# Performance work log

Measured on AMD Instinct MI355X. Metric: run time of the kernel, lower is better.

## Reference

```python
import jax, jax.numpy as jnp
import numpy as np

NUM_HEADS = 8
KERNEL = 7
LOW_RANK = 4


def setup_inputs() -> dict:
    key = jax.random.key(0)
    ks = jax.random.split(key, 10)
    B, H, W, C = 4, 56, 56, 256
    nh, K, lr = NUM_HEADS, KERNEL, LOW_RANK
    s = 0.02
    return {
        "x": jax.random.normal(ks[0], (B, H, W, C), jnp.float32),
        "Wq": jax.random.normal(ks[1], (C, nh * lr), jnp.float32) * s,
        "bq": jnp.zeros((nh * lr,), jnp.float32),
        "Wk": jax.random.normal(ks[2], (C, nh * lr), jnp.float32) * s,
        "bk": jnp.zeros((nh * lr,), jnp.float32),
        "Wv": jax.random.normal(ks[3], (C, C), jnp.float32) * s,
        "bv": jnp.zeros((C,), jnp.float32),
        "rpb": jax.random.normal(ks[4], (nh, 2 * K - 1, 2 * K - 1), jnp.float32) * s,
        "Wp": jax.random.normal(ks[5], (C, C), jnp.float32) * s,
        "bp": jnp.zeros((C,), jnp.float32),
    }


def reference(x, Wq, bq, Wk, bk, Wv, bv, rpb, Wp, bp):
    B, H, W, C = x.shape
    nh, K, lr = NUM_HEADS, KERNEL, LOW_RANK
    hd = C // nh
    r = K // 2
    scale = hd ** -0.5

    # Projections. Note: the original uses a raw reshape (B,H,W,nh*lr)->(B,nh,H,W,lr),
    # which we replicate exactly (row-major reshape, no permute).
    q = (x @ Wq + bq).reshape(B, nh, H, W, lr) * scale
    k = (x @ Wk + bk).reshape(B, nh, H, W, lr)
    v = (x @ Wv + bv).reshape(B, nh, H, W, hd)

    # NATTEN window start indices (clamped so each query sees exactly K keys per axis).
    start_h = jnp.clip(jnp.arange(H) - r, 0, H - K)  # (H,)
    start_w = jnp.clip(jnp.arange(W) - r, 0, W - K)  # (W,)
    idx_h = start_h[:, None] + jnp.arange(K)[None, :]  # (H, K)
    idx_w = start_w[:, None] + jnp.arange(K)[None, :]  # (W, K)

    # Gather local K/V windows: (B, nh, H, K, W, K, d)
    k_win = k[:, :, idx_h][:, :, :, :, idx_w]
    v_win = v[:, :, idx_h][:, :, :, :, idx_w]

    # Scores: (B, nh, H, W, K, K)
    attn = jnp.einsum('bhijc,bhikjlc->bhijkl', q, k_win)

    # Relative position bias indices: (key_pos - query_pos) + (K-1)
    bi = idx_h - jnp.arange(H)[:, None] + (K - 1)  # (H, K)
    bj = idx_w - jnp.arange(W)[:, None] + (K - 1)  # (W, K)
    bias = rpb[:, bi][:, :, :, bj]                 # (nh, H, K, W, K)
    attn = attn + bias.transpose(0, 1, 3, 2, 4)[None]  # (B, nh, H, W, K, K)

    attn = jax.nn.softmax(attn.reshape(B, nh, H, W, K * K), axis=-1)
    attn = attn.reshape(B, nh, H, W, K, K)

    # Weighted aggregation of V windows: (B, nh, H, W, hd)
    out = jnp.einsum('bhijkl,bhikjld->bhijd', attn, v_win)
    out = out.transpose(0, 2, 3, 1, 4).reshape(B, H, W, C)
    return out @ Wp + bp
```

## Files before the change

kernel.cpp:

```cpp
#include <hip/hip_runtime.h>
#include <hip/hip_bf16.h>

#define BD 4
#define HD_ 56
#define WD 56
#define CD 256
#define NH 8
#define KW 7
#define LR 4
#define HDIM 32
#define MB (HD_*WD)
#define NROWS (BD*MB)
#define QK_PER_B (HD_*WD*32)
#define V_PER_B  (HD_*WD*256)

typedef short short8 __attribute__((ext_vector_type(8)));
typedef float floatx4 __attribute__((ext_vector_type(4)));

static __device__ inline ushort f2bf(float f) {
    __hip_bfloat16 h = __float2bfloat16(f);
    return *(ushort*)&h;
}

__global__ __launch_bounds__(256) void prep_w(
    const float* __restrict__ Wq, const float* __restrict__ Wk,
    const float* __restrict__ Wv, const float* __restrict__ bq,
    const float* __restrict__ bk, const float* __restrict__ bv,
    const float* __restrict__ Wp,
    ushort* __restrict__ WpkT, ushort* __restrict__ WpT, float* __restrict__ pb)
{
    int idx = blockIdx.x * 256 + threadIdx.x;
    if (idx < 81920) {
        int n = idx >> 8, k = idx & 255;
        float v;
        if (n < 32)       v = Wq[k * 32 + n];
        else if (n < 64)  v = Wk[k * 32 + (n - 32)];
        else              v = Wv[k * 256 + (n - 64)];
        WpkT[idx] = f2bf(v);
    } else if (idx < 81920 + 65536) {
        int j = idx - 81920;
        int n = j >> 8, k = j & 255;
        WpT[j] = f2bf(Wp[k * 256 + n]);
    } else if (idx < 81920 + 65536 + 320) {
        int n = idx - (81920 + 65536);
        pb[n] = (n < 32) ? bq[n] : (n < 64) ? bk[n - 32] : bv[n - 64];
    }
}

__global__ __launch_bounds__(256) void cvt_x(
    const float* __restrict__ x, ushort* __restrict__ Xb)
{
    int i8 = (blockIdx.x * 256 + threadIdx.x) * 8;
    float4 u = *(const float4*)&x[i8];
    float4 v = *(const float4*)&x[i8 + 4];
    union { ushort h[8]; uint4 q; } pk;
    pk.h[0] = f2bf(u.x); pk.h[1] = f2bf(u.y); pk.h[2] = f2bf(u.z); pk.h[3] = f2bf(u.w);
    pk.h[4] = f2bf(v.x); pk.h[5] = f2bf(v.y); pk.h[6] = f2bf(v.z); pk.h[7] = f2bf(v.w);
    *(uint4*)&Xb[i8] = pk.q;
}

__global__ __launch_bounds__(256) void mfma_qkv(
    const ushort* __restrict__ Ag, const ushort* __restrict__ Bt,
    const float* __restrict__ pb, float* __restrict__ Qb,
    float* __restrict__ Kb, float* __restrict__ Vb)
{
    __shared__ ushort As[64 * 40];
    __shared__ ushort Bs[64 * 40];

    const int t = threadIdx.x;
    const int m0 = blockIdx.y * 64;
    const int n0 = blockIdx.x * 64;
    const int r  = t >> 2;
    const int kq = (t & 3) << 3;
    const int lane = t & 63, w = t >> 6;
    const int col = lane & 15, quad = lane >> 4;
    const int q8 = quad << 3;

    floatx4 acc[4] = {{0,0,0,0},{0,0,0,0},{0,0,0,0},{0,0,0,0}};

    for (int k0 = 0; k0 < 256; k0 += 32) {
        uint4 av = *(const uint4*)&Ag[(m0 + r) * 256 + k0 + kq];
        uint4 bv = *(const uint4*)&Bt[(n0 + r) * 256 + k0 + kq];
        __syncthreads();
        *(uint4*)&As[r * 40 + kq] = av;
        *(uint4*)&Bs[r * 40 + kq] = bv;
        __syncthreads();
        short8 af = *(short8*)&As[((w << 4) + col) * 40 + q8];
#pragma unroll
        for (int nt = 0; nt < 4; ++nt) {
            short8 bf = *(short8*)&Bs[((nt << 4) + col) * 40 + q8];
            acc[nt] = __builtin_amdgcn_mfma_f32_16x16x32_bf16(af, bf, acc[nt], 0, 0, 0);
        }
    }

#pragma unroll
    for (int nt = 0; nt < 4; ++nt) {
        int gn = n0 + (nt << 4) + col;
        float bias = pb[gn];
#pragma unroll
        for (int rg = 0; rg < 4; ++rg) {
            int m = m0 + (w << 4) + (quad << 2) + rg;
            float v = acc[nt][rg] + bias;
            if (n0 == 0 && nt < 2)      Qb[m * 32 + gn] = v;
            else if (n0 == 0)           Kb[m * 32 + (gn - 32)] = v;
            else                        Vb[m * 256 + (gn - 64)] = v;
        }
    }
}

__global__ __launch_bounds__(256) void mfma_out(
    const ushort* __restrict__ Ag, const ushort* __restrict__ Bt,
    const float* __restrict__ bp, float* __restrict__ out)
{
    __shared__ ushort As[64 * 40];
    __shared__ ushort Bs[64 * 40];

    const int t = threadIdx.x;
    const int m0 = blockIdx.y * 64;
    const int n0 = blockIdx.x * 64;
    const int r  = t >> 2;
    const int kq = (t & 3) << 3;
    const int lane = t & 63, w = t >> 6;
    const int col = lane & 15, quad = lane >> 4;
    const int q8 = quad << 3;

    floatx4 acc[4] = {{0,0,0,0},{0,0,0,0},{0,0,0,0},{0,0,0,0}};

    for (int k0 = 0; k0 < 256; k0 += 32) {
        uint4 av = *(const uint4*)&Ag[(m0 + r) * 256 + k0 + kq];
        uint4 bv = *(const uint4*)&Bt[(n0 + r) * 256 + k0 + kq];
        __syncthreads();
        *(uint4*)&As[r * 40 + kq] = av;
        *(uint4*)&Bs[r * 40 + kq] = bv;
        __syncthreads();
        short8 af = *(short8*)&As[((w << 4) + col) * 40 + q8];
#pragma unroll
        for (int nt = 0; nt < 4; ++nt) {
            short8 bf = *(short8*)&Bs[((nt << 4) + col) * 40 + q8];
            acc[nt] = __builtin_amdgcn_mfma_f32_16x16x32_bf16(af, bf, acc[nt], 0, 0, 0);
        }
    }

#pragma unroll
    for (int nt = 0; nt < 4; ++nt) {
        int gn = n0 + (nt << 4) + col;
        float bias = bp[gn];
#pragma unroll
        for (int rg = 0; rg < 4; ++rg) {
            int m = m0 + (w << 4) + (quad << 2) + rg;
            out[m * 256 + gn] = acc[nt][rg] + bias;
        }
    }
}

__global__ __launch_bounds__(256) void natten_attn_t(
    const float* __restrict__ Qb, const float* __restrict__ Kb,
    const float* __restrict__ Vb, const float* __restrict__ rpb,
    ushort* __restrict__ Ab)
{
    __shared__ float4 Ks[196];
    __shared__ float4 Vs[8 * 196];
    __shared__ float  Rs[169];

    const int tj = blockIdx.x, ti = blockIdx.y;
    const int n = blockIdx.z & 7, b = blockIdx.z >> 3;
    const int t = threadIdx.x;
    const int i0 = ti * 8, j0 = tj * 8;
    const int rs = min(max(i0 - 3, 0), HD_ - 14);
    const int cs = min(max(j0 - 3, 0), WD - 14);

    const float* kb = Kb + b * QK_PER_B + n * (HD_ * WD * LR);
    const float* vb = Vb + b * V_PER_B + n * (HD_ * WD * HDIM);

    if (t < 196) {
        int r = t / 14, c = t % 14;
        Ks[t] = *(const float4*)&kb[(rs + r) * (WD * LR) + (cs + c) * LR];
    }
    if (t < 169) Rs[t] = rpb[n * 169 + t];
    for (int idx = t; idx < 1568; idx += 256) {
        int d4 = idx & 7, pos = idx >> 3;
        int r = pos / 14, c = pos % 14;
        Vs[d4 * 196 + pos] = *(const float4*)&vb[(rs + r) * (WD * HDIM) + (cs + c) * HDIM + d4 * 4];
    }
    __syncthreads();

    const int q  = t >> 2, p = t & 3;
    const int qi = q >> 3, qj = q & 7;
    const int i = i0 + qi, j = j0 + qj;
    const int sh = min(max(i - 3, 0), HD_ - KW);
    const int sw = min(max(j - 3, 0), WD - KW);
    const int oh = sh - rs, ow = sw - cs;

    float4 qv = *(const float4*)&Qb[b * QK_PER_B + n * (HD_ * WD * LR) + i * (WD * LR) + j * LR];
    const float scale = 0.17677669529663687f;

    float s[49];
    float mx = -3.4e38f;
#pragma unroll
    for (int kh = 0; kh < KW; ++kh) {
        int rbase = (sh + kh - i + 6) * 13 + (sw - j + 6);
        int kpos  = (oh + kh) * 14 + ow;
#pragma unroll
        for (int kw = 0; kw < KW; ++kw) {
            float4 kv = Ks[kpos + kw];
            float d = qv.x * kv.x + qv.y * kv.y + qv.z * kv.z + qv.w * kv.w;
            float sc = d * scale + Rs[rbase + kw];
            s[kh * KW + kw] = sc;
            mx = fmaxf(mx, sc);
        }
    }
    float sum = 0.f;
#pragma unroll
    for (int pp = 0; pp < 49; ++pp) { float e = __expf(s[pp] - mx); s[pp] = e; sum += e; }
    float inv = 1.0f / sum;

    float4 a0 = {0.f, 0.f, 0.f, 0.f}, a1 = {0.f, 0.f, 0.f, 0.f};
    const float4* v0 = &Vs[(2 * p) * 196];
    const float4* v1 = &Vs[(2 * p + 1) * 196];
#pragma unroll
    for (int kh = 0; kh < KW; ++kh) {
        int kpos = (oh + kh) * 14 + ow;
#pragma unroll
        for (int kw = 0; kw < KW; ++kw) {
            float wt = s[kh * KW + kw] * inv;
            float4 x0 = v0[kpos + kw];
            float4 x1 = v1[kpos + kw];
            a0.x += wt * x0.x; a0.y += wt * x0.y; a0.z += wt * x0.z; a0.w += wt * x0.w;
            a1.x += wt * x1.x; a1.y += wt * x1.y; a1.z += wt * x1.z; a1.w += wt * x1.w;
        }
    }

    union { ushort h[8]; uint4 u; } pk;
    pk.h[0] = f2bf(a0.x); pk.h[1] = f2bf(a0.y); pk.h[2] = f2bf(a0.z); pk.h[3] = f2bf(a0.w);
    pk.h[4] = f2bf(a1.x); pk.h[5] = f2bf(a1.y); pk.h[6] = f2bf(a1.z); pk.h[7] = f2bf(a1.w);
    *(uint4*)&Ab[(((b * HD_ + i) * WD + j)) * CD + n * HDIM + p * 8] = pk.u;
}

extern "C" void kernel_launch(void* const* d_in, const int* in_sizes, int n_in,
                              void* d_out, int out_size, void* d_ws, size_t ws_size,
                              hipStream_t stream) {
    const float* x   = (const float*)d_in[0];
    const float* Wq  = (const float*)d_in[1];
    const float* bq  = (const float*)d_in[2];
    const float* Wk  = (const float*)d_in[3];
    const float* bk  = (const float*)d_in[4];
    const float* Wv  = (const float*)d_in[5];
    const float* bv  = (const float*)d_in[6];
    const float* rpb = (const float*)d_in[7];
    const float* Wp  = (const float*)d_in[8];
    const float* bp  = (const float*)d_in[9];
    float* out = (float*)d_out;

    ushort* WpkT = (ushort*)d_ws;
    ushort* WpT  = WpkT + 81920;
    ushort* Xb   = WpT + 65536;
    ushort* Ab   = Xb + 3211264;
    float*  pb   = (float*)(Ab + 3211264);
    float*  Qb   = pb + 320;
    float*  Kb   = Qb + BD * QK_PER_B;
    float*  Vb   = Kb + BD * QK_PER_B;

    prep_w<<<(81920 + 65536 + 320 + 255) / 256, 256, 0, stream>>>(
        Wq, Wk, Wv, bq, bk, bv, Wp, WpkT, WpT, pb);
    cvt_x<<<(NROWS * CD / 8) / 256, 256, 0, stream>>>(x, Xb);

    mfma_qkv<<<dim3(5, NROWS / 64), 256, 0, stream>>>(Xb, WpkT, pb, Qb, Kb, Vb);

    natten_attn_t<<<dim3(7, 7, 32), 256, 0, stream>>>(Qb, Kb, Vb, rpb, Ab);

    mfma_out<<<dim3(4, NROWS / 64), 256, 0, stream>>>(Ab, WpT, bp, out);
}
```

Measured before the change: 131.3 us.

## Store Q/K/V intermediates in bf16 and merge prep kernels into one launch

The QKV GEMM epilogue now writes Q, K and V as bf16 instead of fp32, and the attention kernel loads, stages in shared memory and unpacks bf16 values. This halves the intermediate traffic between the projection and attention stages and halves the attention kernel's shared memory footprint. The weight-prep and x-conversion kernels are also merged into a single launch to save one launch overhead. It adds bf16 rounding to Q/K/V, which may reduce accuracy.

After: 140.7 us. 1.07x slower.

```diff
diff --git a/kernel.cpp b/kernel.cpp
--- a/kernel.cpp
+++ b/kernel.cpp
@@ -21,48 +21,55 @@
     __hip_bfloat16 h = __float2bfloat16(f);
     return *(ushort*)&h;
 }
-
-__global__ __launch_bounds__(256) void prep_w(
+static __device__ inline float bf2f(uint h16) {
+    union { uint u; float f; } c; c.u = h16 << 16; return c.f;
+}
+static __device__ inline float bf2f_hi(uint u) {
+    union { uint v; float f; } c; c.v = u & 0xffff0000u; return c.f;
+}
+
+__global__ __launch_bounds__(256) void prep_all(
+    const float* __restrict__ x,
     const float* __restrict__ Wq, const float* __restrict__ Wk,
     const float* __restrict__ Wv, const float* __restrict__ bq,
     const float* __restrict__ bk, const float* __restrict__ bv,
     const float* __restrict__ Wp,
-    ushort* __restrict__ WpkT, ushort* __restrict__ WpT, float* __restrict__ pb)
-{
-    int idx = blockIdx.x * 256 + threadIdx.x;
-    if (idx < 81920) {
-        int n = idx >> 8, k = idx & 255;
-        float v;
-        if (n < 32)       v = Wq[k * 32 + n];
-        else if (n < 64)  v = Wk[k * 32 + (n - 32)];
-        else              v = Wv[k * 256 + (n - 64)];
-        WpkT[idx] = f2bf(v);
-    } else if (idx < 81920 + 65536) {
-        int j = idx - 81920;
-        int n = j >> 8, k = j & 255;
-        WpT[j] = f2bf(Wp[k * 256 + n]);
-    } else if (idx < 81920 + 65536 + 320) {
-        int n = idx - (81920 + 65536);
-        pb[n] = (n < 32) ? bq[n] : (n < 64) ? bk[n - 32] : bv[n - 64];
-    }
-}
-
-__global__ __launch_bounds__(256) void cvt_x(
-    const float* __restrict__ x, ushort* __restrict__ Xb)
-{
-    int i8 = (blockIdx.x * 256 + threadIdx.x) * 8;
-    float4 u = *(const float4*)&x[i8];
-    float4 v = *(const float4*)&x[i8 + 4];
-    union { ushort h[8]; uint4 q; } pk;
-    pk.h[0] = f2bf(u.x); pk.h[1] = f2bf(u.y); pk.h[2] = f2bf(u.z); pk.h[3] = f2bf(u.w);
-    pk.h[4] = f2bf(v.x); pk.h[5] = f2bf(v.y); pk.h[6] = f2bf(v.z); pk.h[7] = f2bf(v.w);
-    *(uint4*)&Xb[i8] = pk.q;
+    ushort* __restrict__ Xb, ushort* __restrict__ WpkT,
+    ushort* __restrict__ WpT, float* __restrict__ pb)
+{
+    int blk = blockIdx.x;
+    if (blk < 1568) {
+        int i8 = (blk * 256 + threadIdx.x) * 8;
+        float4 u = *(const float4*)&x[i8];
+        float4 v = *(const float4*)&x[i8 + 4];
+        union { ushort h[8]; uint4 q; } pk;
+        pk.h[0] = f2bf(u.x); pk.h[1] = f2bf(u.y); pk.h[2] = f2bf(u.z); pk.h[3] = f2bf(u.w);
+        pk.h[4] = f2bf(v.x); pk.h[5] = f2bf(v.y); pk.h[6] = f2bf(v.z); pk.h[7] = f2bf(v.w);
+        *(uint4*)&Xb[i8] = pk.q;
+    } else {
+        int idx = (blk - 1568) * 256 + threadIdx.x;
+        if (idx < 81920) {
+            int n = idx >> 8, k = idx & 255;
+            float v;
+            if (n < 32)       v = Wq[k * 32 + n];
+            else if (n < 64)  v = Wk[k * 32 + (n - 32)];
+            else              v = Wv[k * 256 + (n - 64)];
+            WpkT[idx] = f2bf(v);
+        } else if (idx < 81920 + 65536) {
+            int j = idx - 81920;
+            int n = j >> 8, k = j & 255;
+            WpT[j] = f2bf(Wp[k * 256 + n]);
+        } else if (idx < 81920 + 65536 + 320) {
+            int n = idx - (81920 + 65536);
+            pb[n] = (n < 32) ? bq[n] : (n < 64) ? bk[n - 32] : bv[n - 64];
+        }
+    }
 }
 
 __global__ __launch_bounds__(256) void mfma_qkv(
     const ushort* __restrict__ Ag, const ushort* __restrict__ Bt,
-    const float* __restrict__ pb, float* __restrict__ Qb,
-    float* __restrict__ Kb, float* __restrict__ Vb)
+    const float* __restrict__ pb, ushort* __restrict__ Qb,
+    ushort* __restrict__ Kb, ushort* __restrict__ Vb)
 {
     __shared__ ushort As[64 * 40];
     __shared__ ushort Bs[64 * 40];
@@ -100,10 +107,10 @@
 #pragma unroll
         for (int rg = 0; rg < 4; ++rg) {
             int m = m0 + (w << 4) + (quad << 2) + rg;
-            float v = acc[nt][rg] + bias;
-            if (n0 == 0 && nt < 2)      Qb[m * 32 + gn] = v;
-            else if (n0 == 0)           Kb[m * 32 + (gn - 32)] = v;
-            else                        Vb[m * 256 + (gn - 64)] = v;
+            ushort h = f2bf(acc[nt][rg] + bias);
+            if (n0 == 0 && nt < 2)      Qb[m * 32 + gn] = h;
+            else if (n0 == 0)           Kb[m * 32 + (gn - 32)] = h;
+            else                        Vb[m * 256 + (gn - 64)] = h;
         }
     }
 }
@@ -154,12 +161,12 @@
 }
 
 __global__ __launch_bounds__(256) void natten_attn_t(
-    const float* __restrict__ Qb, const float* __restrict__ Kb,
-    const float* __restrict__ Vb, const float* __restrict__ rpb,
+    const ushort* __restrict__ Qb, const ushort* __restrict__ Kb,
+    const ushort* __restrict__ Vb, const float* __restrict__ rpb,
     ushort* __restrict__ Ab)
 {
-    __shared__ float4 Ks[196];
-    __shared__ float4 Vs[8 * 196];
+    __shared__ ushort Ks[196 * 4];
+    __shared__ ushort Vs[4 * 196 * 8];
     __shared__ float  Rs[169];
 
     const int tj = blockIdx.x, ti = blockIdx.y;
@@ -169,18 +176,19 @@
     const int rs = min(max(i0 - 3, 0), HD_ - 14);
     const int cs = min(max(j0 - 3, 0), WD - 14);
 
-    const float* kb = Kb + b * QK_PER_B + n * (HD_ * WD * LR);
-    const float* vb = Vb + b * V_PER_B + n * (HD_ * WD * HDIM);
+    const ushort* kb = Kb + b * QK_PER_B + n * (HD_ * WD * LR);
+    const ushort* vb = Vb + b * V_PER_B + n * (HD_ * WD * HDIM);
 
     if (t < 196) {
         int r = t / 14, c = t % 14;
-        Ks[t] = *(const float4*)&kb[(rs + r) * (WD * LR) + (cs + c) * LR];
+        *(uint2*)&Ks[t * 4] = *(const uint2*)&kb[(rs + r) * (WD * LR) + (cs + c) * LR];
     }
     if (t < 169) Rs[t] = rpb[n * 169 + t];
-    for (int idx = t; idx < 1568; idx += 256) {
-        int d4 = idx & 7, pos = idx >> 3;
+    for (int idx = t; idx < 784; idx += 256) {
+        int oct = idx & 3, pos = idx >> 2;
         int r = pos / 14, c = pos % 14;
-        Vs[d4 * 196 + pos] = *(const float4*)&vb[(rs + r) * (WD * HDIM) + (cs + c) * HDIM + d4 * 4];
+        *(uint4*)&Vs[(oct * 196 + pos) * 8] =
+            *(const uint4*)&vb[(rs + r) * (WD * HDIM) + (cs + c) * HDIM + oct * 8];
     }
     __syncthreads();
 
@@ -191,7 +199,10 @@
     const int sw = min(max(j - 3, 0), WD - KW);
     const int oh = sh - rs, ow = sw - cs;
 
-    float4 qv = *(const float4*)&Qb[b * QK_PER_B + n * (HD_ * WD * LR) + i * (WD * LR) + j * LR];
+    union { uint2 u; uint w[2]; } qr;
+    qr.u = *(const uint2*)&Qb[b * QK_PER_B + n * (HD_ * WD * LR) + i * (WD * LR) + j * LR];
+    float qx = bf2f(qr.w[0] & 0xffff), qy = bf2f_hi(qr.w[0]);
+    float qz = bf2f(qr.w[1] & 0xffff), qw = bf2f_hi(qr.w[1]);
     const float scale = 0.17677669529663687f;
 
     float s[49];
@@ -202,8 +213,10 @@
         int kpos  = (oh + kh) * 14 + ow;
 #pragma unroll
         for (int kw = 0; kw < KW; ++kw) {
-            float4 kv = Ks[kpos + kw];
-            float d = qv.x * kv.x + qv.y * kv.y + qv.z * kv.z + qv.w * kv.w;
+            union { uint2 u; uint w[2]; } kr;
+            kr.u = *(const uint2*)&Ks[(kpos + kw) * 4];
+            float d = qx * bf2f(kr.w[0] & 0xffff) + qy * bf2f_hi(kr.w[0])
+                    + qz * bf2f(kr.w[1] & 0xffff) + qw * bf2f_hi(kr.w[1]);
             float sc = d * scale + Rs[rbase + kw];
             s[kh * KW + kw] = sc;
             mx = fmaxf(mx, sc);
@@ -214,25 +227,27 @@
     for (int pp = 0; pp < 49; ++pp) { float e = __expf(s[pp] - mx); s[pp] = e; sum += e; }
     float inv = 1.0f / sum;
 
-    float4 a0 = {0.f, 0.f, 0.f, 0.f}, a1 = {0.f, 0.f, 0.f, 0.f};
-    const float4* v0 = &Vs[(2 * p) * 196];
-    const float4* v1 = &Vs[(2 * p + 1) * 196];
+    float a[8] = {0.f, 0.f, 0.f, 0.f, 0.f, 0.f, 0.f, 0.f};
+    const ushort* vsl = &Vs[p * (196 * 8)];
 #pragma unroll
     for (int kh = 0; kh < KW; ++kh) {
         int kpos = (oh + kh) * 14 + ow;
 #pragma unroll
         for (int kw = 0; kw < KW; ++kw) {
             float wt = s[kh * KW + kw] * inv;
-            float4 x0 = v0[kpos + kw];
-            float4 x1 = v1[kpos + kw];
-            a0.x += wt * x0.x; a0.y += wt * x0.y; a0.z += wt * x0.z; a0.w += wt * x0.w;
-            a1.x += wt * x1.x; a1.y += wt * x1.y; a1.z += wt * x1.z; a1.w += wt * x1.w;
+            union { uint4 u; uint w[4]; } vr;
+            vr.u = *(const uint4*)&vsl[(kpos + kw) * 8];
+#pragma unroll
+            for (int c = 0; c < 4; ++c) {
+                a[2 * c]     += wt * bf2f(vr.w[c] & 0xffff);
+                a[2 * c + 1] += wt * bf2f_hi(vr.w[c]);
+            }
         }
     }
 
     union { ushort h[8]; uint4 u; } pk;
-    pk.h[0] = f2bf(a0.x); pk.h[1] = f2bf(a0.y); pk.h[2] = f2bf(a0.z); pk.h[3] = f2bf(a0.w);
-    pk.h[4] = f2bf(a1.x); pk.h[5] = f2bf(a1.y); pk.h[6] = f2bf(a1.z); pk.h[7] = f2bf(a1.w);
+#pragma unroll
+    for (int c = 0; c < 8; ++c) pk.h[c] = f2bf(a[c]);
     *(uint4*)&Ab[(((b * HD_ + i) * WD + j)) * CD + n * HDIM + p * 8] = pk.u;
 }
 
@@ -255,14 +270,13 @@
     ushort* WpT  = WpkT + 81920;
     ushort* Xb   = WpT + 65536;
     ushort* Ab   = Xb + 3211264;
-    float*  pb   = (float*)(Ab + 3211264);
-    float*  Qb   = pb + 320;
-    float*  Kb   = Qb + BD * QK_PER_B;
-    float*  Vb   = Kb + BD * QK_PER_B;
-
-    prep_w<<<(81920 + 65536 + 320 + 255) / 256, 256, 0, stream>>>(
-        Wq, Wk, Wv, bq, bk, bv, Wp, WpkT, WpT, pb);
-    cvt_x<<<(NROWS * CD / 8) / 256, 256, 0, stream>>>(x, Xb);
+    ushort* Qb   = Ab + 3211264;
+    ushort* Kb   = Qb + BD * QK_PER_B;
+    ushort* Vb   = Kb + BD * QK_PER_B;
+    float*  pb   = (float*)(Vb + BD * V_PER_B);
+
+    prep_all<<<1568 + 578, 256, 0, stream>>>(
+        x, Wq, Wk, Wv, bq, bk, bv, Wp, Xb, WpkT, WpT, pb);
 
     mfma_qkv<<<dim3(5, NROWS / 64), 256, 0, stream>>>(Xb, WpkT, pb, Qb, Kb, Vb);
 
```
